# Optimization experiments

Hardware: AMD Instinct MI355X
Metric: run time of the kernel (lower is better)

Reference implementation:

```python
import jax, jax.numpy as jnp
import numpy as np

K = 8          # knn_graph default k
LOW = 64       # low_res_size
FIRE = 0.5     # fire_rate
HID = 16       # hidden_channels
HEADS = 4      # GAT heads
OUTC = HID // HEADS  # per-head out channels = 4
EPS = 1e-5


def conv3x3(x, W, b):
    y = jax.lax.conv_general_dilated(x, W, (1, 1), 'SAME',
                                     dimension_numbers=('NCHW', 'OIHW', 'NCHW'))
    return y + b[None, :, None, None]


def bnorm(x, g, b, m, v):
    scale = (g / jnp.sqrt(v + EPS))[None, :, None, None]
    return (x - m[None, :, None, None]) * scale + b[None, :, None, None]


def conv1x1(x, W, b):  # W: [out, in]
    return jnp.einsum('bchw,oc->bohw', x, W) + b[None, :, None, None]


def gat_image(nodes, Wg, a_src, a_dst, bg):
    # nodes: [N, HID]. kNN graph (loop=False) + GATConv with self-loops added.
    N = nodes.shape[0]
    sq = jnp.sum(nodes * nodes, axis=1)
    D = sq[:, None] + sq[None, :] - 2.0 * (nodes @ nodes.T)
    D = jax.lax.stop_gradient(D) + jnp.eye(N, dtype=nodes.dtype) * 1e9  # exclude self
    idx = jax.lax.top_k(-D, K)[1]                                   # [N, K] nearest nbrs
    nbr = jnp.concatenate([idx, jnp.arange(N)[:, None]], axis=1)    # [N, K+1] + self-loop
    xp = (nodes @ Wg.T).reshape(N, HEADS, OUTC)                     # [N, H, F]
    asr = jnp.sum(xp * a_src[None], axis=-1)                        # [N, H]
    adt = jnp.sum(xp * a_dst[None], axis=-1)                        # [N, H]
    logits = jax.nn.leaky_relu(asr[nbr] + adt[:, None, :], 0.2)     # [N, K+1, H]
    att = jax.nn.softmax(logits, axis=1)                            # softmax over incoming edges
    out = jnp.sum(att[..., None] * xp[nbr], axis=1)                 # [N, H, F]
    out = out.reshape(N, HEADS * OUTC) + bg
    return jax.nn.relu(out)                                         # GrapherModule relu


def setup_inputs() -> dict:
    key = jax.random.key(0)
    ks = jax.random.split(key, 24)
    f = jnp.float32
    d = {}
    d['x'] = jax.random.normal(ks[0], (8, 1, 256, 256), f)
    d['fire_rand'] = jax.random.uniform(ks[1], (8, 1, LOW, LOW), f)
    # encoder_b1: conv(1->64,3) BN conv(64->16,3) BN
    d['W1'] = jax.random.normal(ks[2], (64, 1, 3, 3), f) * 0.2
    d['b1'] = jax.random.normal(ks[3], (64,), f) * 0.05
    d['g1'] = jnp.ones((64,), f); d['be1'] = jnp.zeros((64,), f)
    d['m1'] = jax.random.normal(ks[4], (64,), f) * 0.1
    d['v1'] = jax.random.uniform(ks[5], (64,), f) + 0.5
    d['W2'] = jax.random.normal(ks[6], (HID, 64, 3, 3), f) * 0.05
    d['b2'] = jax.random.normal(ks[7], (HID,), f) * 0.05
    d['g2'] = jnp.ones((HID,), f); d['be2'] = jnp.zeros((HID,), f)
    d['m2'] = jax.random.normal(ks[8], (HID,), f) * 0.1
    d['v2'] = jax.random.uniform(ks[9], (HID,), f) + 0.5
    # GATConv(16 -> 4 per head, heads=4)
    d['Wg'] = jax.random.normal(ks[10], (HEADS * OUTC, HID), f) * 0.25
    d['a_src'] = jax.random.normal(ks[11], (HEADS, OUTC), f) * 0.5
    d['a_dst'] = jax.random.normal(ks[12], (HEADS, OUTC), f) * 0.5
    d['bg'] = jax.random.normal(ks[13], (HEADS * OUTC,), f) * 0.05
    # update_net_b1: 1x1 conv 16->128->16
    d['Wu1'] = jax.random.normal(ks[14], (128, HID), f) * 0.25
    d['bu1'] = jax.random.normal(ks[15], (128,), f) * 0.05
    d['Wu2'] = jax.random.normal(ks[16], (HID, 128), f) * 0.08
    d['bu2'] = jax.random.normal(ks[17], (HID,), f) * 0.05
    # to_output_b1: 1x1 conv 16->1
    d['Wo'] = jax.random.normal(ks[18], (1, HID), f) * 0.25
    d['bo'] = jax.random.normal(ks[19], (1,), f) * 0.05
    return d


def reference(x, fire_rand, W1, b1, g1, be1, m1, v1, W2, b2, g2, be2, m2, v2,
              Wg, a_src, a_dst, bg, Wu1, bu1, Wu2, bu2, Wo, bo):
    B, C, H, W = x.shape
    xl = jax.image.resize(x, (B, C, LOW, LOW), 'bilinear')
    h = jax.nn.relu(bnorm(conv3x3(xl, W1, b1), g1, be1, m1, v1))
    h = jax.nn.relu(bnorm(conv3x3(h, W2, b2), g2, be2, m2, v2))
    # one NCA step: graph process -> update net -> stochastic fire mask
    N = LOW * LOW
    nodes = h.reshape(B, HID, N).transpose(0, 2, 1)            # [B, N, HID]
    p = jax.vmap(gat_image, in_axes=(0, None, None, None, None))(nodes, Wg, a_src, a_dst, bg)
    p = p.transpose(0, 2, 1).reshape(B, HID, LOW, LOW)
    u = conv1x1(jax.nn.relu(conv1x1(p, Wu1, bu1)), Wu2, bu2)
    mask = (fire_rand < FIRE).astype(h.dtype)                   # [B,1,LOW,LOW]
    h = h + mask * u
    out = jax.nn.sigmoid(conv1x1(h, Wo, bo))
    return jax.image.resize(out, (B, C, H, W), 'bilinear')
```

## Files before the change

### kernel.cpp

```cpp
#include <hip/hip_runtime.h>
#include <math.h>
#include <float.h>

#define BATCH 8
#define HIGH  256
#define LOWR  64
#define NN    4096
#define HIDC  16
#define C1    64
#define NSL   8

#define OFF_XL   0
#define OFF_H1   (OFF_XL  + BATCH*NN)
#define OFF_H    (OFF_H1  + BATCH*C1*NN)
#define OFF_SQ   (OFF_H   + BATCH*NN*HIDC)
#define OFF_XP   (OFF_SQ  + BATCH*NN)
#define OFF_ASR  (OFF_XP  + BATCH*NN*HIDC)
#define OFF_ADT  (OFF_ASR + BATCH*NN*4)
#define OFF_P    (OFF_ADT + BATCH*NN*4)
#define OFF_OL   (OFF_P   + BATCH*NN*HIDC)

typedef __attribute__((ext_vector_type(8)))  short bf16x8;
typedef __attribute__((ext_vector_type(16))) float f32x16;

__device__ __forceinline__ float dot16m(const float ni[16], float4 a0, float4 a1,
                                        float4 a2, float4 a3, float hs) {
    return ni[0]*a0.x + ni[1]*a0.y + ni[2]*a0.z + ni[3]*a0.w
         + ni[4]*a1.x + ni[5]*a1.y + ni[6]*a1.z + ni[7]*a1.w
         + ni[8]*a2.x + ni[9]*a2.y + ni[10]*a2.z + ni[11]*a2.w
         + ni[12]*a3.x + ni[13]*a3.y + ni[14]*a3.z + ni[15]*a3.w
         - hs;
}

__global__ void k_down(const float* __restrict__ x, float* __restrict__ xl) {
    int t = blockIdx.x * 128 + threadIdx.x;
    if (t >= BATCH * NN) return;
    int b = t >> 12, oy = (t >> 6) & 63, ox = t & 63;
    const float* xb = x + b * HIGH * HIGH;
    float cy = 4.f * oy + 1.5f, cx = 4.f * ox + 1.5f;
    float wy[8], wx[8], sy = 0.f, sx = 0.f;
#pragma unroll
    for (int k = 0; k < 8; k++) {
        int iy = 4 * oy - 2 + k;
        float w = 1.f - fabsf((float)iy - cy) * 0.25f;
        if (iy < 0 || iy >= HIGH) w = 0.f;
        wy[k] = w; sy += w;
        int ix = 4 * ox - 2 + k;
        float v = 1.f - fabsf((float)ix - cx) * 0.25f;
        if (ix < 0 || ix >= HIGH) v = 0.f;
        wx[k] = v; sx += v;
    }
    float acc = 0.f;
#pragma unroll
    for (int ky = 0; ky < 8; ky++) {
        if (wy[ky] == 0.f) continue;
        int iy = 4 * oy - 2 + ky;
        float rowacc = 0.f;
#pragma unroll
        for (int kx = 0; kx < 8; kx++) {
            if (wx[kx] == 0.f) continue;
            int ix = 4 * ox - 2 + kx;
            rowacc += wx[kx] * xb[iy * HIGH + ix];
        }
        acc += wy[ky] * rowacc;
    }
    xl[t] = acc / (sy * sx);
}

__global__ void k_conv1(const float* __restrict__ xl, const float* __restrict__ W1,
                        const float* __restrict__ b1, const float* __restrict__ g1,
                        const float* __restrict__ be1, const float* __restrict__ m1,
                        const float* __restrict__ v1, float* __restrict__ h1) {
    int t = blockIdx.x * 256 + threadIdx.x;
    if (t >= BATCH * C1 * NN) return;
    int b = t >> 18, co = (t >> 12) & 63, y = (t >> 6) & 63, x = t & 63;
    const float* src = xl + b * NN;
    const float* w = W1 + co * 9;
    float acc = 0.f;
#pragma unroll
    for (int dy = -1; dy <= 1; dy++) {
        int yy = y + dy; if (yy < 0 || yy >= 64) continue;
#pragma unroll
        for (int dx = -1; dx <= 1; dx++) {
            int xx = x + dx; if (xx < 0 || xx >= 64) continue;
            acc += w[(dy + 1) * 3 + (dx + 1)] * src[yy * 64 + xx];
        }
    }
    acc += b1[co];
    float sc = g1[co] / sqrtf(v1[co] + 1e-5f);
    acc = (acc - m1[co]) * sc + be1[co];
    h1[t] = fmaxf(acc, 0.f);
}

__launch_bounds__(512)
__global__ void k_conv2(const float* __restrict__ h1, const float* __restrict__ W2,
                        const float* __restrict__ b2, const float* __restrict__ g2,
                        const float* __restrict__ be2, const float* __restrict__ m2,
                        const float* __restrict__ v2, const float* __restrict__ Wg,
                        const float* __restrict__ a_src, const float* __restrict__ a_dst,
                        float* __restrict__ h, float* __restrict__ sq,
                        float* __restrict__ xp, float* __restrict__ asr,
                        float* __restrict__ adt) {
    __shared__ float sW2t[576 * 16];
    __shared__ float sWg[256];
    __shared__ float sA[32];
    __shared__ float accH[3][128][17];
    int tid = threadIdx.x;
    for (int k = tid; k < 9216; k += 512) {
        int o = k / 576, ct = k - o * 576;
        sW2t[ct * 16 + o] = W2[k];
    }
    if (tid < 256) sWg[tid] = Wg[tid];
    if (tid < 16) { sA[tid] = a_src[tid]; sA[16 + tid] = a_dst[tid]; }
    __syncthreads();
    int blk = blockIdx.x;
    int b = blk >> 5, ytile = blk & 31;
    int q = tid >> 7;
    int sub = tid & 127;
    int ty = sub >> 6, x = sub & 63, y = ytile * 2 + ty;
    float acc[16];
#pragma unroll
    for (int o = 0; o < 16; o++) acc[o] = 0.f;
    const float* hb = h1 + (long)b * C1 * NN + (long)q * 16 * NN;
    for (int ci = 0; ci < 16; ci++) {
        const float* plane = hb + ci * NN;
#pragma unroll
        for (int dy = -1; dy <= 1; dy++) {
            int yy = y + dy; bool oky = (yy >= 0 && yy < 64);
#pragma unroll
            for (int dx = -1; dx <= 1; dx++) {
                int xx = x + dx;
                float v = (oky && xx >= 0 && xx < 64) ? plane[yy * 64 + xx] : 0.f;
                int ct = (q * 16 + ci) * 9 + (dy + 1) * 3 + (dx + 1);
                const float4* wr = (const float4*)&sW2t[ct * 16];
                float4 w0 = wr[0], w1 = wr[1], w2 = wr[2], w3 = wr[3];
                acc[0] += v * w0.x; acc[1] += v * w0.y; acc[2] += v * w0.z; acc[3] += v * w0.w;
                acc[4] += v * w1.x; acc[5] += v * w1.y; acc[6] += v * w1.z; acc[7] += v * w1.w;
                acc[8] += v * w2.x; acc[9] += v * w2.y; acc[10]+= v * w2.z; acc[11]+= v * w2.w;
                acc[12]+= v * w3.x; acc[13]+= v * w3.y; acc[14]+= v * w3.z; acc[15]+= v * w3.w;
            }
        }
    }
    if (q != 0) {
        float* dst = &accH[q - 1][sub][0];
#pragma unroll
        for (int o = 0; o < 16; o++) dst[o] = acc[o];
    }
    __syncthreads();
    if (q != 0) return;
#pragma unroll
    for (int qq = 0; qq < 3; qq++) {
        const float* src = &accH[qq][sub][0];
#pragma unroll
        for (int o = 0; o < 16; o++) acc[o] += src[o];
    }
    int n = y * 64 + x;
    long node = (long)b * NN + n;
    float nodev[16], sqv = 0.f;
#pragma unroll
    for (int o = 0; o < 16; o++) {
        float a = acc[o] + b2[o];
        float sc = g2[o] / sqrtf(v2[o] + 1e-5f);
        a = (a - m2[o]) * sc + be2[o];
        a = fmaxf(a, 0.f);
        nodev[o] = a; sqv += a * a;
        h[node * 16 + o] = a;
    }
    sq[node] = 0.5f * sqv;
    float xpv[16];
#pragma unroll
    for (int o = 0; o < 16; o++) {
        float a = 0.f;
#pragma unroll
        for (int c = 0; c < 16; c++) a += sWg[o * 16 + c] * nodev[c];
        xpv[o] = a;
        xp[node * 16 + o] = a;
    }
#pragma unroll
    for (int hh = 0; hh < 4; hh++) {
        float as = 0.f, ad = 0.f;
#pragma unroll
        for (int f = 0; f < 4; f++) {
            as += xpv[hh * 4 + f] * sA[hh * 4 + f];
            ad += xpv[hh * 4 + f] * sA[16 + hh * 4 + f];
        }
        asr[node * 4 + hh] = as;
        adt[node * 4 + hh] = ad;
    }
}

__device__ __forceinline__ ushort f2bf(float f) {
    unsigned u = __float_as_uint(f);
    return (ushort)((u + 0x7FFFu + ((u >> 16) & 1u)) >> 16);
}
__device__ __forceinline__ float bf2f(ushort h) {
    return __uint_as_float(((unsigned)h) << 16);
}
__global__ void k_split(const float* __restrict__ h, const float* __restrict__ sq,
                        ushort* __restrict__ hHi, ushort* __restrict__ hMid,
                        ushort* __restrict__ hLo, float* __restrict__ nsq) {
    long t = (long)blockIdx.x * 64 + threadIdx.x;
    nsq[t] = -sq[t];
    const float4* hp = (const float4*)&h[t * 16];
    float4 v0 = hp[0], v1 = hp[1], v2 = hp[2], v3 = hp[3];
    float v[16] = { v0.x,v0.y,v0.z,v0.w, v1.x,v1.y,v1.z,v1.w,
                    v2.x,v2.y,v2.z,v2.w, v3.x,v3.y,v3.z,v3.w };
    unsigned wh[8], wm[8], wl[8];
#pragma unroll
    for (int p = 0; p < 8; p++) {
        unsigned packh = 0, packm = 0, packl = 0;
#pragma unroll
        for (int e = 0; e < 2; e++) {
            float f = v[p * 2 + e];
            ushort hi = f2bf(f);
            float t1 = f - bf2f(hi);
            ushort mi = f2bf(t1);
            float t2 = t1 - bf2f(mi);
            ushort lo = f2bf(t2);
            packh |= ((unsigned)hi) << (16 * e);
            packm |= ((unsigned)mi) << (16 * e);
            packl |= ((unsigned)lo) << (16 * e);
        }
        wh[p] = packh; wm[p] = packm; wl[p] = packl;
    }
    uint4* dh = (uint4*)&hHi[t * 16];
    uint4* dm = (uint4*)&hMid[t * 16];
    uint4* dl = (uint4*)&hLo[t * 16];
    dh[0] = make_uint4(wh[0], wh[1], wh[2], wh[3]);
    dh[1] = make_uint4(wh[4], wh[5], wh[6], wh[7]);
    dm[0] = make_uint4(wm[0], wm[1], wm[2], wm[3]);
    dm[1] = make_uint4(wm[4], wm[5], wm[6], wm[7]);
    dl[0] = make_uint4(wl[0], wl[1], wl[2], wl[3]);
    dl[1] = make_uint4(wl[4], wl[5], wl[6], wl[7]);
}

__device__ __forceinline__ void tile_scores(const ushort* __restrict__ hHi,
        const ushort* __restrict__ hMid, const ushort* __restrict__ hLo,
        const float* __restrict__ nsq, long bN, int j0, int ln31, int koff,
        int rbase, int i0w, bf16x8 bi_h, bf16x8 bi_m, bf16x8 bi_l,
        float scv[16]) {
    int jr = j0 + ln31;
    bf16x8 aj_h = *(const bf16x8*)&hHi [(bN + jr) * 16 + koff];
    bf16x8 aj_m = *(const bf16x8*)&hMid[(bN + jr) * 16 + koff];
    bf16x8 aj_l = *(const bf16x8*)&hLo [(bN + jr) * 16 + koff];
    float4 q0 = *(const float4*)&nsq[bN + j0 +  0 + rbase];
    float4 q1 = *(const float4*)&nsq[bN + j0 +  8 + rbase];
    float4 q2 = *(const float4*)&nsq[bN + j0 + 16 + rbase];
    float4 q3 = *(const float4*)&nsq[bN + j0 + 24 + rbase];
    f32x16 acc;
    acc[0]  = q0.x; acc[1]  = q0.y; acc[2]  = q0.z; acc[3]  = q0.w;
    acc[4]  = q1.x; acc[5]  = q1.y; acc[6]  = q1.z; acc[7]  = q1.w;
    acc[8]  = q2.x; acc[9]  = q2.y; acc[10] = q2.z; acc[11] = q2.w;
    acc[12] = q3.x; acc[13] = q3.y; acc[14] = q3.z; acc[15] = q3.w;
    acc = __builtin_amdgcn_mfma_f32_32x32x16_bf16(aj_h, bi_h, acc, 0, 0, 0);
    acc = __builtin_amdgcn_mfma_f32_32x32x16_bf16(aj_h, bi_m, acc, 0, 0, 0);
    acc = __builtin_amdgcn_mfma_f32_32x32x16_bf16(aj_m, bi_h, acc, 0, 0, 0);
    acc = __builtin_amdgcn_mfma_f32_32x32x16_bf16(aj_h, bi_l, acc, 0, 0, 0);
    acc = __builtin_amdgcn_mfma_f32_32x32x16_bf16(aj_l, bi_h, acc, 0, 0, 0);
    acc = __builtin_amdgcn_mfma_f32_32x32x16_bf16(aj_m, bi_m, acc, 0, 0, 0);
#pragma unroll
    for (int rr = 0; rr < 16; rr++) scv[rr] = acc[rr];
    if (j0 == i0w) {
#pragma unroll
        for (int rr = 0; rr < 16; rr++) {
            int r = (rr & 3) + 8 * (rr >> 2) + rbase;
            if (r == ln31) scv[rr] = -FLT_MAX;
        }
    }
}

#define CEX(a, b) { float ce_hi = fmaxf(a, b), ce_lo = fminf(a, b); (a) = ce_hi; (b) = ce_lo; }
__device__ __forceinline__ void sort8d(float v[8]) {
    CEX(v[0],v[1]); CEX(v[2],v[3]); CEX(v[4],v[5]); CEX(v[6],v[7]);
    CEX(v[0],v[2]); CEX(v[1],v[3]); CEX(v[4],v[6]); CEX(v[5],v[7]);
    CEX(v[1],v[2]); CEX(v[5],v[6]);
    CEX(v[0],v[4]); CEX(v[1],v[5]); CEX(v[2],v[6]); CEX(v[3],v[7]);
    CEX(v[2],v[4]); CEX(v[3],v[5]);
    CEX(v[1],v[2]); CEX(v[3],v[4]); CEX(v[5],v[6]);
}
__device__ __forceinline__ void bsort8d(float v[8]) {
    CEX(v[0],v[4]); CEX(v[1],v[5]); CEX(v[2],v[6]); CEX(v[3],v[7]);
    CEX(v[0],v[2]); CEX(v[1],v[3]); CEX(v[4],v[6]); CEX(v[5],v[7]);
    CEX(v[0],v[1]); CEX(v[2],v[3]); CEX(v[4],v[5]); CEX(v[6],v[7]);
}
#define CEX2(sa, ia, sb, ib) { \
    bool sw2 = ((sb) > (sa)) || ((sb) == (sa) && (ib) < (ia)); \
    float th2 = sw2 ? (sb) : (sa); float tl2 = sw2 ? (sa) : (sb); \
    int   ih2 = sw2 ? (ib) : (ia); int   il2 = sw2 ? (ia) : (ib); \
    (sa) = th2; (sb) = tl2; (ia) = ih2; (ib) = il2; }
__device__ __forceinline__ void bsort8d_id(float v[8], int id[8]) {
    CEX2(v[0],id[0],v[4],id[4]); CEX2(v[1],id[1],v[5],id[5]);
    CEX2(v[2],id[2],v[6],id[6]); CEX2(v[3],id[3],v[7],id[7]);
    CEX2(v[0],id[0],v[2],id[2]); CEX2(v[1],id[1],v[3],id[3]);
    CEX2(v[4],id[4],v[6],id[6]); CEX2(v[5],id[5],v[7],id[7]);
    CEX2(v[0],id[0],v[1],id[1]); CEX2(v[2],id[2],v[3],id[3]);
    CEX2(v[4],id[4],v[5],id[5]); CEX2(v[6],id[6],v[7],id[7]);
}

__global__ __attribute__((amdgpu_waves_per_eu(4, 8))) __launch_bounds__(256)
void k_scan(const ushort* __restrict__ hHi, const ushort* __restrict__ hMid,
            const ushort* __restrict__ hLo, const float* __restrict__ nsq,
            uint4* __restrict__ cand_i) {
    __shared__ ushort lists[256][18];
    __shared__ ushort outl[256][8];
    int tid = threadIdx.x, blk = blockIdx.x;
    int b  = blk >> 8;
    int ig = (blk >> 3) & 31;
    int sl = blk & 7;
    int wid = tid >> 6, lane = tid & 63;
    int ln31 = lane & 31, l5 = lane >> 5;
    int koff = l5 * 8;
    int i0w = ig * 128 + wid * 32;
    int i   = i0w + ln31;
    long bN = (long)b * NN;
    int rbase = l5 * 4;
    int jbase = sl * 512;

    bf16x8 bi_h = *(const bf16x8*)&hHi [(bN + i) * 16 + koff];
    bf16x8 bi_m = *(const bf16x8*)&hMid[(bN + i) * 16 + koff];
    bf16x8 bi_l = *(const bf16x8*)&hLo [(bN + i) * 16 + koff];

    float s[8];
#pragma unroll
    for (int k = 0; k < 8; k++) s[k] = -FLT_MAX;
#pragma unroll 2
    for (int t = 0; t < 16; t++) {
        int j0 = jbase + t * 32;
        float scv[16];
        tile_scores(hHi, hMid, hLo, nsq, bN, j0, ln31, koff, rbase, i0w,
                    bi_h, bi_m, bi_l, scv);
        float va[8] = { scv[0], scv[1], scv[2], scv[3], scv[4], scv[5], scv[6], scv[7] };
        float vb[8] = { scv[8], scv[9], scv[10], scv[11], scv[12], scv[13], scv[14], scv[15] };
        sort8d(va); sort8d(vb);
        float mg[8];
#pragma unroll
        for (int k = 0; k < 8; k++) mg[k] = fmaxf(va[k], vb[7 - k]);
        bsort8d(mg);
#pragma unroll
        for (int k = 0; k < 8; k++) s[k] = fmaxf(s[k], mg[7 - k]);
        bsort8d(s);
    }
    float mv[8];
#pragma unroll
    for (int k = 0; k < 8; k++) mv[k] = fmaxf(s[k], __shfl_xor(s[7 - k], 32));
    float theta = mv[0];
#pragma unroll
    for (int k = 1; k < 8; k++) theta = fminf(theta, mv[k]);

    ushort* ldsw = &lists[0][0];
    int baseA = tid * 18, baseB = baseA + 8, trash = baseA + 16;
    int nA = 0, nB = 0;
#pragma unroll 2
    for (int t = 0; t < 16; t++) {
        int j0 = jbase + t * 32;
        float scv[16];
        tile_scores(hHi, hMid, hLo, nsq, bN, j0, ln31, koff, rbase, i0w,
                    bi_h, bi_m, bi_l, scv);
        unsigned gm = 0, em = 0;
#pragma unroll
        for (int rr = 0; rr < 16; rr++) {
            gm |= (scv[rr] >  theta) ? (1u << rr) : 0u;
            em |= (scv[rr] == theta) ? (1u << rr) : 0u;
        }
        unsigned m = gm | em;
        while (__any(m != 0u)) {
            if (m) {
                int rr = __ffs(m) - 1;
                m &= m - 1u;
                int r = (rr & 3) + ((rr >> 2) << 3) + rbase;
                int j = j0 + r;
                bool isGt = (gm >> rr) & 1u;
                bool cA = isGt && (nA < 8);
                bool cB = (!isGt) && (nB < 8);
                int ia = cA ? (baseA + nA) : (cB ? (baseB + nB) : trash);
                ldsw[ia] = (ushort)j;
                nA += cA;
                nB += cB;
            }
        }
    }
    int pA = __shfl_xor(nA, 32);
    int pB = __shfl_xor(nB, 32);
    __syncthreads();
    if (lane < 32) {
        int tp = tid + 32;
        int n = 0;
        for (int k = 0; k < nA && n < 8; k++) outl[tid][n++] = lists[tid][k];
        for (int k = 0; k < pA && n < 8; k++) outl[tid][n++] = lists[tp][k];
        int p0 = 0, p1 = 0;
        while (n < 8) {
            unsigned a = (p0 < nB) ? (unsigned)lists[tid][8 + p0] : 0xFFFFFFFFu;
            unsigned c = (p1 < pB) ? (unsigned)lists[tp][8 + p1] : 0xFFFFFFFFu;
            bool t0 = a < c;
            outl[tid][n++] = (ushort)(t0 ? a : c);
            p0 += t0 ? 1 : 0; p1 += t0 ? 0 : 1;
        }
        uint4 pk = *(const uint4*)&outl[tid][0];
        cand_i[(long)(b * NSL + sl) * NN + i] = pk;
    }
}

__launch_bounds__(64)
__global__ void k_gat2(const uint4* __restrict__ cand_i, const float* __restrict__ h,
                       const float* __restrict__ sq,
                       const float* __restrict__ xp, const float* __restrict__ asr,
                       const float* __restrict__ adt, const float* __restrict__ bg,
                       float* __restrict__ p) {
    int lane = threadIdx.x;
    int ln15 = lane & 15, q = lane >> 4;
    int t = blockIdx.x * 16 + ln15;
    int b = t >> 12, i = t & 4095;
    long bN = (long)b * NN;
    const float4* ip = (const float4*)&h[(bN + i) * 16];
    float4 r0 = ip[0], r1 = ip[1], r2 = ip[2], r3 = ip[3];
    float ni[16] = { r0.x,r0.y,r0.z,r0.w, r1.x,r1.y,r1.z,r1.w,
                     r2.x,r2.y,r2.z,r2.w, r3.x,r3.y,r3.z,r3.w };
    float fS[8]; int fI[8];
#pragma unroll
    for (int k = 0; k < 8; k++) { fS[k] = -FLT_MAX; fI[k] = 65535; }
#pragma unroll
    for (int ss = 0; ss < 2; ss++) {
        int sl = q * 2 + ss;
        uint4 pk = cand_i[(long)(b * NSL + sl) * NN + i];
        unsigned idx8[8] = { pk.x & 0xFFFF, pk.x >> 16, pk.y & 0xFFFF, pk.y >> 16,
                             pk.z & 0xFFFF, pk.z >> 16, pk.w & 0xFFFF, pk.w >> 16 };
#pragma unroll
        for (int k = 0; k < 8; k++) {
            int j = (int)idx8[k];
            const float4* np = (const float4*)&h[(bN + j) * 16];
            float4 a0 = np[0], a1 = np[1], a2 = np[2], a3 = np[3];
            float d = dot16m(ni, a0, a1, a2, a3, sq[bN + j]);
            bool bt = (d > fS[7]) || (d == fS[7] && j < fI[7]);
            if (bt) {
                fS[7] = d; fI[7] = j;
#pragma unroll
                for (int qq = 7; qq > 0; qq--) {
                    bool sw = (fS[qq] > fS[qq - 1]) || (fS[qq] == fS[qq - 1] && fI[qq] < fI[qq - 1]);
                    if (sw) {
                        float td = fS[qq]; fS[qq] = fS[qq - 1]; fS[qq - 1] = td;
                        int tj = fI[qq]; fI[qq] = fI[qq - 1]; fI[qq - 1] = tj;
                    }
                }
            }
        }
    }
    float oS[8]; int oI[8];
#pragma unroll
    for (int k = 0; k < 8; k++) {
        oS[k] = __shfl_xor(fS[k], 16);
        oI[k] = __shfl_xor(fI[k], 16);
    }
    float mS[8]; int mI[8];
#pragma unroll
    for (int k = 0; k < 8; k++) {
        bool mine = (fS[k] > oS[7 - k]) || (fS[k] == oS[7 - k] && fI[k] < oI[7 - k]);
        mS[k] = mine ? fS[k] : oS[7 - k];
        mI[k] = mine ? fI[k] : oI[7 - k];
    }
    bsort8d_id(mS, mI);
#pragma unroll
    for (int k = 0; k < 8; k++) {
        oS[k] = __shfl_xor(mS[k], 32);
        oI[k] = __shfl_xor(mI[k], 32);
    }
    int nI[8];
#pragma unroll
    for (int k = 0; k < 8; k++) {
        bool mine = (mS[k] > oS[7 - k]) || (mS[k] == oS[7 - k] && mI[k] < oI[7 - k]);
        nI[k] = mine ? mI[k] : oI[7 - k];
    }
    if (q != 0) return;
    int nbrs[9];
#pragma unroll
    for (int e = 0; e < 8; e++) nbrs[e] = nI[e];
    nbrs[8] = i;
    float adtv[4];
#pragma unroll
    for (int hh = 0; hh < 4; hh++) adtv[hh] = adt[(bN + i) * 4 + hh];
    float mx[4] = { -FLT_MAX, -FLT_MAX, -FLT_MAX, -FLT_MAX };
    float lg[9][4];
#pragma unroll
    for (int e = 0; e < 9; e++) {
        long nb = bN + nbrs[e];
#pragma unroll
        for (int hh = 0; hh < 4; hh++) {
            float l = asr[nb * 4 + hh] + adtv[hh];
            l = (l > 0.f) ? l : 0.2f * l;
            lg[e][hh] = l;
            mx[hh] = fmaxf(mx[hh], l);
        }
    }
    float sum[4] = { 0, 0, 0, 0 };
    float acc[16];
#pragma unroll
    for (int c = 0; c < 16; c++) acc[c] = 0.f;
#pragma unroll
    for (int e = 0; e < 9; e++) {
        long nb = bN + nbrs[e];
        const float4* xpn = (const float4*)&xp[nb * 16];
        float4 x0 = xpn[0], x1 = xpn[1], x2 = xpn[2], x3 = xpn[3];
        float xv[16] = { x0.x,x0.y,x0.z,x0.w, x1.x,x1.y,x1.z,x1.w,
                         x2.x,x2.y,x2.z,x2.w, x3.x,x3.y,x3.z,x3.w };
        float wv[4];
#pragma unroll
        for (int hh = 0; hh < 4; hh++) {
            float w = expf(lg[e][hh] - mx[hh]);
            sum[hh] += w; wv[hh] = w;
        }
#pragma unroll
        for (int hh = 0; hh < 4; hh++)
#pragma unroll
            for (int f = 0; f < 4; f++)
                acc[hh * 4 + f] += wv[hh] * xv[hh * 4 + f];
    }
#pragma unroll
    for (int hh = 0; hh < 4; hh++) {
        float inv = 1.f / sum[hh];
#pragma unroll
        for (int f = 0; f < 4; f++) {
            float o = acc[hh * 4 + f] * inv + bg[hh * 4 + f];
            p[(bN + i) * 16 + hh * 4 + f] = fmaxf(o, 0.f);
        }
    }
}

__launch_bounds__(256)
__global__ void k_update(const float* __restrict__ p, const float* __restrict__ h,
                         const float* __restrict__ fire, const float* __restrict__ Wu1,
                         const float* __restrict__ bu1, const float* __restrict__ Wu2,
                         const float* __restrict__ bu2, const float* __restrict__ Wo,
                         const float* __restrict__ bo, float* __restrict__ out_low) {
    __shared__ float sU1[128 * 16];
    __shared__ float sU2t[128 * 16];
    __shared__ float sb1[128];
    __shared__ float upart[3][64][17];
    int tid = threadIdx.x;
    for (int k = tid; k < 2048; k += 256) {
        sU1[k] = Wu1[k];
        sU2t[(k & 127) * 16 + (k >> 7)] = Wu2[k];
    }
    if (tid < 128) sb1[tid] = bu1[tid];
    __syncthreads();
    int lnode = tid & 63, q = tid >> 6;
    long n = (long)blockIdx.x * 64 + lnode;
    const float4* pp = (const float4*)&p[n * 16];
    float4 p0 = pp[0], p1 = pp[1], p2 = pp[2], p3 = pp[3];
    float pv[16] = { p0.x,p0.y,p0.z,p0.w, p1.x,p1.y,p1.z,p1.w,
                     p2.x,p2.y,p2.z,p2.w, p3.x,p3.y,p3.z,p3.w };
    float u[16];
#pragma unroll
    for (int c = 0; c < 16; c++) u[c] = 0.f;
    int hd0 = q * 32;
    for (int hd = hd0; hd < hd0 + 32; hd++) {
        const float4* r = (const float4*)&sU1[hd * 16];
        float4 r0 = r[0], r1 = r[1], r2 = r[2], r3 = r[3];
        float a = sb1[hd]
            + r0.x*pv[0] + r0.y*pv[1] + r0.z*pv[2] + r0.w*pv[3]
            + r1.x*pv[4] + r1.y*pv[5] + r1.z*pv[6] + r1.w*pv[7]
            + r2.x*pv[8] + r2.y*pv[9] + r2.z*pv[10]+ r2.w*pv[11]
            + r3.x*pv[12]+ r3.y*pv[13]+ r3.z*pv[14]+ r3.w*pv[15];
        a = fmaxf(a, 0.f);
        const float4* tt = (const float4*)&sU2t[hd * 16];
        float4 t0 = tt[0], t1 = tt[1], t2 = tt[2], t3 = tt[3];
        u[0] += t0.x*a; u[1] += t0.y*a; u[2] += t0.z*a; u[3] += t0.w*a;
        u[4] += t1.x*a; u[5] += t1.y*a; u[6] += t1.z*a; u[7] += t1.w*a;
        u[8] += t2.x*a; u[9] += t2.y*a; u[10]+= t2.z*a; u[11]+= t2.w*a;
        u[12]+= t3.x*a; u[13]+= t3.y*a; u[14]+= t3.z*a; u[15]+= t3.w*a;
    }
    if (q != 0) {
        float* dst = &upart[q - 1][lnode][0];
#pragma unroll
        for (int c = 0; c < 16; c++) dst[c] = u[c];
    }
    __syncthreads();
    if (q != 0) return;
#pragma unroll
    for (int qq = 0; qq < 3; qq++) {
        const float* src = &upart[qq][lnode][0];
#pragma unroll
        for (int c = 0; c < 16; c++) u[c] += src[c];
    }
    float mask = (fire[n] < 0.5f) ? 1.f : 0.f;
    const float4* hp = (const float4*)&h[n * 16];
    float4 h0 = hp[0], h1v = hp[1], h2 = hp[2], h3 = hp[3];
    float hv[16] = { h0.x,h0.y,h0.z,h0.w, h1v.x,h1v.y,h1v.z,h1v.w,
                     h2.x,h2.y,h2.z,h2.w, h3.x,h3.y,h3.z,h3.w };
    float o = bo[0];
#pragma unroll
    for (int c = 0; c < 16; c++)
        o += Wo[c] * (hv[c] + mask * (u[c] + bu2[c]));
    out_low[n] = 1.f / (1.f + expf(-o));
}

__global__ void k_up(const float* __restrict__ ol, float* __restrict__ out) {
    int t = blockIdx.x * 256 + threadIdx.x;
    if (t >= BATCH * HIGH * HIGH) return;
    int b = t >> 16, oy = (t >> 8) & 255, ox = t & 255;
    float cy = (oy + 0.5f) * 0.25f - 0.5f;
    float cx = (ox + 0.5f) * 0.25f - 0.5f;
    int iy0 = (int)floorf(cy); float fy = cy - (float)iy0;
    int ix0 = (int)floorf(cx); float fx = cx - (float)ix0;
    int y0 = min(max(iy0, 0), 63), y1 = min(max(iy0 + 1, 0), 63);
    int x0 = min(max(ix0, 0), 63), x1 = min(max(ix0 + 1, 0), 63);
    const float* s = ol + b * NN;
    float v = (1.f - fy) * ((1.f - fx) * s[y0 * 64 + x0] + fx * s[y0 * 64 + x1])
            + fy * ((1.f - fx) * s[y1 * 64 + x0] + fx * s[y1 * 64 + x1]);
    out[t] = v;
}

extern "C" void kernel_launch(void* const* d_in, const int* in_sizes, int n_in,
                              void* d_out, int out_size, void* d_ws, size_t ws_size,
                              hipStream_t stream) {
    const float* x    = (const float*)d_in[0];
    const float* fire = (const float*)d_in[1];
    const float* W1   = (const float*)d_in[2];
    const float* b1   = (const float*)d_in[3];
    const float* g1   = (const float*)d_in[4];
    const float* be1  = (const float*)d_in[5];
    const float* m1   = (const float*)d_in[6];
    const float* v1   = (const float*)d_in[7];
    const float* W2   = (const float*)d_in[8];
    const float* b2   = (const float*)d_in[9];
    const float* g2   = (const float*)d_in[10];
    const float* be2  = (const float*)d_in[11];
    const float* m2   = (const float*)d_in[12];
    const float* v2   = (const float*)d_in[13];
    const float* Wg   = (const float*)d_in[14];
    const float* a_src= (const float*)d_in[15];
    const float* a_dst= (const float*)d_in[16];
    const float* bg   = (const float*)d_in[17];
    const float* Wu1  = (const float*)d_in[18];
    const float* bu1  = (const float*)d_in[19];
    const float* Wu2  = (const float*)d_in[20];
    const float* bu2  = (const float*)d_in[21];
    const float* Wo   = (const float*)d_in[22];
    const float* bo   = (const float*)d_in[23];

    float* ws  = (float*)d_ws;
    float* xl  = ws + OFF_XL;
    float* h1  = ws + OFF_H1;
    float* h   = ws + OFF_H;
    float* sq  = ws + OFF_SQ;
    float* xp  = ws + OFF_XP;
    float* asr = ws + OFF_ASR;
    float* adt = ws + OFF_ADT;
    float* p   = ws + OFF_P;
    float* ol  = ws + OFF_OL;
    uint4*  cand_i = (uint4*)(ws + OFF_H1);
    ushort* hHi    = (ushort*)(ws + OFF_H1 + 1048576);
    ushort* hMid   = (ushort*)(ws + OFF_H1 + 1310720);
    ushort* hLo    = (ushort*)(ws + OFF_H1 + 1572864);
    float*  nsq    = ws + OFF_H1 + 1835008;

    k_down  <<<(BATCH * NN + 127) / 128, 128, 0, stream>>>(x, xl);
    k_conv1 <<<(BATCH * C1 * NN) / 256, 256, 0, stream>>>(xl, W1, b1, g1, be1, m1, v1, h1);
    k_conv2 <<<BATCH * 32, 512, 0, stream>>>(h1, W2, b2, g2, be2, m2, v2, Wg, a_src, a_dst,
                                             h, sq, xp, asr, adt);
    k_split <<<BATCH * NN / 64, 64, 0, stream>>>(h, sq, hHi, hMid, hLo, nsq);
    k_scan  <<<BATCH * 32 * NSL, 256, 0, stream>>>(hHi, hMid, hLo, nsq, cand_i);
    k_gat2  <<<BATCH * NN / 16, 64, 0, stream>>>(cand_i, h, sq, xp, asr, adt, bg, p);
    k_update<<<BATCH * NN / 64, 256, 0, stream>>>(p, h, fire, Wu1, bu1, Wu2, bu2, Wo, bo, ol);
    k_up    <<<(BATCH * HIGH * HIGH) / 256, 256, 0, stream>>>(ol, (float*)d_out);
}
```

Baseline: 277.1 us.

## Fuse GAT aggregation with update MLP and output projection in one kernel

Merges k_update into k_gat2. The GAT output p is passed through shared memory instead of global memory. The hidden-channel MLP is split across the four 16-lane groups and reduced with cross-lane shuffles, and the node's own h features already held in registers are reused. This removes one kernel launch and the p write and read round trip. In exchange, every 64-thread block now reloads the 2048-element weight matrices into shared memory, which is 2048 blocks each loading about 16KB.

```diff
diff --git a/kernel.cpp b/kernel.cpp
--- a/kernel.cpp
+++ b/kernel.cpp
@@ -405,8 +405,21 @@
                        const float* __restrict__ sq,
                        const float* __restrict__ xp, const float* __restrict__ asr,
                        const float* __restrict__ adt, const float* __restrict__ bg,
-                       float* __restrict__ p) {
+                       const float* __restrict__ fire, const float* __restrict__ Wu1,
+                       const float* __restrict__ bu1, const float* __restrict__ Wu2,
+                       const float* __restrict__ bu2, const float* __restrict__ Wo,
+                       const float* __restrict__ bo, float* __restrict__ out_low) {
+    __shared__ float sU1[128 * 16];
+    __shared__ float sU2t[128 * 16];
+    __shared__ float sb1[128];
+    __shared__ float pshare[16][17];
     int lane = threadIdx.x;
+    for (int k = lane; k < 2048; k += 64) {
+        sU1[k] = Wu1[k];
+        sU2t[(k & 127) * 16 + (k >> 7)] = Wu2[k];
+    }
+    sb1[lane] = bu1[lane];
+    sb1[lane + 64] = bu1[lane + 64];
     int ln15 = lane & 15, q = lane >> 4;
     int t = blockIdx.x * 16 + ln15;
     int b = t >> 12, i = t & 4095;
@@ -469,96 +482,76 @@
         bool mine = (mS[k] > oS[7 - k]) || (mS[k] == oS[7 - k] && mI[k] < oI[7 - k]);
         nI[k] = mine ? mI[k] : oI[7 - k];
     }
-    if (q != 0) return;
-    int nbrs[9];
-#pragma unroll
-    for (int e = 0; e < 8; e++) nbrs[e] = nI[e];
-    nbrs[8] = i;
-    float adtv[4];
-#pragma unroll
-    for (int hh = 0; hh < 4; hh++) adtv[hh] = adt[(bN + i) * 4 + hh];
-    float mx[4] = { -FLT_MAX, -FLT_MAX, -FLT_MAX, -FLT_MAX };
-    float lg[9][4];
-#pragma unroll
-    for (int e = 0; e < 9; e++) {
-        long nb = bN + nbrs[e];
+    if (q == 0) {
+        int nbrs[9];
+#pragma unroll
+        for (int e = 0; e < 8; e++) nbrs[e] = nI[e];
+        nbrs[8] = i;
+        float adtv[4];
+#pragma unroll
+        for (int hh = 0; hh < 4; hh++) adtv[hh] = adt[(bN + i) * 4 + hh];
+        float mx[4] = { -FLT_MAX, -FLT_MAX, -FLT_MAX, -FLT_MAX };
+        float lg[9][4];
+#pragma unroll
+        for (int e = 0; e < 9; e++) {
+            long nb = bN + nbrs[e];
+#pragma unroll
+            for (int hh = 0; hh < 4; hh++) {
+                float l = asr[nb * 4 + hh] + adtv[hh];
+                l = (l > 0.f) ? l : 0.2f * l;
+                lg[e][hh] = l;
+                mx[hh] = fmaxf(mx[hh], l);
+            }
+        }
+        float sum[4] = { 0, 0, 0, 0 };
+        float acc[16];
+#pragma unroll
+        for (int c = 0; c < 16; c++) acc[c] = 0.f;
+#pragma unroll
+        for (int e = 0; e < 9; e++) {
+            long nb = bN + nbrs[e];
+            const float4* xpn = (const float4*)&xp[nb * 16];
+            float4 x0 = xpn[0], x1 = xpn[1], x2 = xpn[2], x3 = xpn[3];
+            float xv[16] = { x0.x,x0.y,x0.z,x0.w, x1.x,x1.y,x1.z,x1.w,
+                             x2.x,x2.y,x2.z,x2.w, x3.x,x3.y,x3.z,x3.w };
+            float wv[4];
+#pragma unroll
+            for (int hh = 0; hh < 4; hh++) {
+                float w = expf(lg[e][hh] - mx[hh]);
+                sum[hh] += w; wv[hh] = w;
+            }
+#pragma unroll
+            for (int hh = 0; hh < 4; hh++)
+#pragma unroll
+                for (int f = 0; f < 4; f++)
+                    acc[hh * 4 + f] += wv[hh] * xv[hh * 4 + f];
+        }
 #pragma unroll
         for (int hh = 0; hh < 4; hh++) {
-            float l = asr[nb * 4 + hh] + adtv[hh];
-            l = (l > 0.f) ? l : 0.2f * l;
-            lg[e][hh] = l;
-            mx[hh] = fmaxf(mx[hh], l);
-        }
-    }
-    float sum[4] = { 0, 0, 0, 0 };
-    float acc[16];
-#pragma unroll
-    for (int c = 0; c < 16; c++) acc[c] = 0.f;
-#pragma unroll
-    for (int e = 0; e < 9; e++) {
-        long nb = bN + nbrs[e];
-        const float4* xpn = (const float4*)&xp[nb * 16];
-        float4 x0 = xpn[0], x1 = xpn[1], x2 = xpn[2], x3 = xpn[3];
-        float xv[16] = { x0.x,x0.y,x0.z,x0.w, x1.x,x1.y,x1.z,x1.w,
-                         x2.x,x2.y,x2.z,x2.w, x3.x,x3.y,x3.z,x3.w };
-        float wv[4];
-#pragma unroll
-        for (int hh = 0; hh < 4; hh++) {
-            float w = expf(lg[e][hh] - mx[hh]);
-            sum[hh] += w; wv[hh] = w;
-        }
-#pragma unroll
-        for (int hh = 0; hh < 4; hh++)
-#pragma unroll
-            for (int f = 0; f < 4; f++)
-                acc[hh * 4 + f] += wv[hh] * xv[hh * 4 + f];
-    }
-#pragma unroll
-    for (int hh = 0; hh < 4; hh++) {
-        float inv = 1.f / sum[hh];
-#pragma unroll
-        for (int f = 0; f < 4; f++) {
-            float o = acc[hh * 4 + f] * inv + bg[hh * 4 + f];
-            p[(bN + i) * 16 + hh * 4 + f] = fmaxf(o, 0.f);
-        }
-    }
-}
-
-__launch_bounds__(256)
-__global__ void k_update(const float* __restrict__ p, const float* __restrict__ h,
-                         const float* __restrict__ fire, const float* __restrict__ Wu1,
-                         const float* __restrict__ bu1, const float* __restrict__ Wu2,
-                         const float* __restrict__ bu2, const float* __restrict__ Wo,
-                         const float* __restrict__ bo, float* __restrict__ out_low) {
-    __shared__ float sU1[128 * 16];
-    __shared__ float sU2t[128 * 16];
-    __shared__ float sb1[128];
-    __shared__ float upart[3][64][17];
-    int tid = threadIdx.x;
-    for (int k = tid; k < 2048; k += 256) {
-        sU1[k] = Wu1[k];
-        sU2t[(k & 127) * 16 + (k >> 7)] = Wu2[k];
-    }
-    if (tid < 128) sb1[tid] = bu1[tid];
+            float inv = 1.f / sum[hh];
+#pragma unroll
+            for (int f = 0; f < 4; f++) {
+                float o = acc[hh * 4 + f] * inv + bg[hh * 4 + f];
+                pshare[ln15][hh * 4 + f] = fmaxf(o, 0.f);
+            }
+        }
+    }
     __syncthreads();
-    int lnode = tid & 63, q = tid >> 6;
-    long n = (long)blockIdx.x * 64 + lnode;
-    const float4* pp = (const float4*)&p[n * 16];
-    float4 p0 = pp[0], p1 = pp[1], p2 = pp[2], p3 = pp[3];
-    float pv[16] = { p0.x,p0.y,p0.z,p0.w, p1.x,p1.y,p1.z,p1.w,
-                     p2.x,p2.y,p2.z,p2.w, p3.x,p3.y,p3.z,p3.w };
+    float pv[16];
+#pragma unroll
+    for (int c = 0; c < 16; c++) pv[c] = pshare[ln15][c];
     float u[16];
 #pragma unroll
     for (int c = 0; c < 16; c++) u[c] = 0.f;
     int hd0 = q * 32;
     for (int hd = hd0; hd < hd0 + 32; hd++) {
         const float4* r = (const float4*)&sU1[hd * 16];
-        float4 r0 = r[0], r1 = r[1], r2 = r[2], r3 = r[3];
+        float4 w0 = r[0], w1 = r[1], w2 = r[2], w3 = r[3];
         float a = sb1[hd]
-            + r0.x*pv[0] + r0.y*pv[1] + r0.z*pv[2] + r0.w*pv[3]
-            + r1.x*pv[4] + r1.y*pv[5] + r1.z*pv[6] + r1.w*pv[7]
-            + r2.x*pv[8] + r2.y*pv[9] + r2.z*pv[10]+ r2.w*pv[11]
-            + r3.x*pv[12]+ r3.y*pv[13]+ r3.z*pv[14]+ r3.w*pv[15];
+            + w0.x*pv[0] + w0.y*pv[1] + w0.z*pv[2] + w0.w*pv[3]
+            + w1.x*pv[4] + w1.y*pv[5] + w1.z*pv[6] + w1.w*pv[7]
+            + w2.x*pv[8] + w2.y*pv[9] + w2.z*pv[10]+ w2.w*pv[11]
+            + w3.x*pv[12]+ w3.y*pv[13]+ w3.z*pv[14]+ w3.w*pv[15];
         a = fmaxf(a, 0.f);
         const float4* tt = (const float4*)&sU2t[hd * 16];
         float4 t0 = tt[0], t1 = tt[1], t2 = tt[2], t3 = tt[3];
@@ -567,29 +560,19 @@
         u[8] += t2.x*a; u[9] += t2.y*a; u[10]+= t2.z*a; u[11]+= t2.w*a;
         u[12]+= t3.x*a; u[13]+= t3.y*a; u[14]+= t3.z*a; u[15]+= t3.w*a;
     }
-    if (q != 0) {
-        float* dst = &upart[q - 1][lnode][0];
-#pragma unroll
-        for (int c = 0; c < 16; c++) dst[c] = u[c];
-    }
-    __syncthreads();
-    if (q != 0) return;
-#pragma unroll
-    for (int qq = 0; qq < 3; qq++) {
-        const float* src = &upart[qq][lnode][0];
-#pragma unroll
-        for (int c = 0; c < 16; c++) u[c] += src[c];
-    }
-    float mask = (fire[n] < 0.5f) ? 1.f : 0.f;
-    const float4* hp = (const float4*)&h[n * 16];
-    float4 h0 = hp[0], h1v = hp[1], h2 = hp[2], h3 = hp[3];
-    float hv[16] = { h0.x,h0.y,h0.z,h0.w, h1v.x,h1v.y,h1v.z,h1v.w,
-                     h2.x,h2.y,h2.z,h2.w, h3.x,h3.y,h3.z,h3.w };
-    float o = bo[0];
-#pragma unroll
-    for (int c = 0; c < 16; c++)
-        o += Wo[c] * (hv[c] + mask * (u[c] + bu2[c]));
-    out_low[n] = 1.f / (1.f + expf(-o));
+#pragma unroll
+    for (int c = 0; c < 16; c++) {
+        u[c] += __shfl_xor(u[c], 16);
+        u[c] += __shfl_xor(u[c], 32);
+    }
+    if (q == 0) {
+        float mask = (fire[t] < 0.5f) ? 1.f : 0.f;
+        float o = bo[0];
+#pragma unroll
+        for (int c = 0; c < 16; c++)
+            o += Wo[c] * (ni[c] + mask * (u[c] + bu2[c]));
+        out_low[t] = 1.f / (1.f + expf(-o));
+    }
 }
 
 __global__ void k_up(const float* __restrict__ ol, float* __restrict__ out) {
@@ -644,7 +627,6 @@
     float* xp  = ws + OFF_XP;
     float* asr = ws + OFF_ASR;
     float* adt = ws + OFF_ADT;
-    float* p   = ws + OFF_P;
     float* ol  = ws + OFF_OL;
     uint4*  cand_i = (uint4*)(ws + OFF_H1);
     ushort* hHi    = (ushort*)(ws + OFF_H1 + 1048576);
@@ -658,7 +640,7 @@
                                              h, sq, xp, asr, adt);
     k_split <<<BATCH * NN / 64, 64, 0, stream>>>(h, sq, hHi, hMid, hLo, nsq);
     k_scan  <<<BATCH * 32 * NSL, 256, 0, stream>>>(hHi, hMid, hLo, nsq, cand_i);
-    k_gat2  <<<BATCH * NN / 16, 64, 0, stream>>>(cand_i, h, sq, xp, asr, adt, bg, p);
-    k_update<<<BATCH * NN / 64, 256, 0, stream>>>(p, h, fire, Wu1, bu1, Wu2, bu2, Wo, bo, ol);
+    k_gat2  <<<BATCH * NN / 16, 64, 0, stream>>>(cand_i, h, sq, xp, asr, adt, bg,
+                                                 fire, Wu1, bu1, Wu2, bu2, Wo, bo, ol);
     k_up    <<<(BATCH * HIGH * HIGH) / 256, 256, 0, stream>>>(ol, (float*)d_out);
 }
```

Measured after the change: 271.2 us. 1.02x faster.
